# Optimization experiments

Hardware: AMD Instinct MI355X
Metric: run time of the kernel (lower is better)

## Reference

```python
import jax, jax.numpy as jnp
import numpy as np

N = 64000   # nodes
E = 256000  # edges
G = 2000    # graphs
D = 300     # emb_dim
H = 4       # heads
C = D // H  # head dim = 75
L = 5       # layers
ED = 32     # edge_emb_dim
FD = 256    # feat_dim


def _ln(x, g, b):
    m = x.mean(-1, keepdims=True)
    v = jnp.mean((x - m) ** 2, axis=-1, keepdims=True)
    return (x - m) * jax.lax.rsqrt(v + 1e-5) * g + b


def setup_inputs() -> dict:
    key = jax.random.key(0)
    ks = iter(jax.random.split(key, 48))
    def nrm(shape, s=0.02):
        return jax.random.normal(next(ks), shape, jnp.float32) * s
    inp = {}
    inp["x"] = jax.random.randint(next(ks), (N, 2), 0, 3)
    inp["edge_index"] = jax.random.randint(next(ks), (2, E), 0, N)
    inp["edge_attr"] = jax.random.randint(next(ks), (E, 2), 0, 3)
    inp["batch"] = jnp.sort(jax.random.randint(next(ks), (N,), 0, G))
    inp.update(dict(
        x_emb1=nrm((119, D)), x_emb2=nrm((3, D)),
        e_emb_t=nrm((5, ED)), e_emb_d=nrm((3, ED)),
        edge_proj_w=nrm((ED, ED)), edge_proj_b=nrm((ED,)),
        q_w=nrm((L, D, D)), q_b=nrm((L, D)),
        k_w=nrm((L, D, D)), k_b=nrm((L, D)),
        v_w=nrm((L, D, D)), v_b=nrm((L, D)),
        e_w=nrm((L, ED, D)),
        skip_w=nrm((L, D, D)), skip_b=nrm((L, D)),
        ln1_g=jnp.ones((L, D), jnp.float32), ln1_b=jnp.zeros((L, D), jnp.float32),
        ln2_g=jnp.ones((L, D), jnp.float32), ln2_b=jnp.zeros((L, D), jnp.float32),
        ffn_w1=nrm((L, D, 4 * D)), ffn_b1=nrm((L, 4 * D)),
        ffn_w2=nrm((L, 4 * D, D)), ffn_b2=nrm((L, D)),
        feat_w=nrm((D, FD)), feat_b=nrm((FD,)),
        out_w1=nrm((FD, FD)), out_b1=nrm((FD,)),
        out_w2=nrm((FD, FD // 2)), out_b2=nrm((FD // 2,)),
    ))
    return inp


def reference(x, edge_index, edge_attr, batch, x_emb1, x_emb2, e_emb_t, e_emb_d,
              edge_proj_w, edge_proj_b, q_w, q_b, k_w, k_b, v_w, v_b, e_w,
              skip_w, skip_b, ln1_g, ln1_b, ln2_g, ln2_b,
              ffn_w1, ffn_b1, ffn_w2, ffn_b2, feat_w, feat_b,
              out_w1, out_b1, out_w2, out_b2):
    # node / edge embeddings
    h = x_emb1[x[:, 0]] + x_emb2[x[:, 1]]                               # [N, D]
    ef = (e_emb_t[edge_attr[:, 0]] + e_emb_d[edge_attr[:, 1]]) @ edge_proj_w + edge_proj_b  # [E, ED]
    src, dst = edge_index[0], edge_index[1]
    scale = 1.0 / np.sqrt(C).astype(np.float32)
    for l in range(L):  # loop over fixed layer count
        q = (h @ q_w[l] + q_b[l]).reshape(N, H, C)
        k = (h @ k_w[l] + k_b[l]).reshape(N, H, C)
        v = (h @ v_w[l] + v_b[l]).reshape(N, H, C)
        e = (ef @ e_w[l]).reshape(E, H, C)
        kj = k[src] + e                                                 # [E, H, C]
        alpha = jnp.einsum('ehc,ehc->eh', q[dst], kj) * scale           # [E, H]
        amax = jax.lax.stop_gradient(jax.ops.segment_max(alpha, dst, num_segments=N))
        ea = jnp.exp(alpha - amax[dst])
        den = jax.ops.segment_sum(ea, dst, num_segments=N)
        attn = ea / den[dst]                                            # segment softmax over in-edges of dst
        msg = attn[:, :, None] * (v[src] + e)
        agg = jax.ops.segment_sum(msg, dst, num_segments=N).reshape(N, D)
        conv = agg + h @ skip_w[l] + skip_b[l]                          # TransformerConv with root skip
        h = _ln(h + conv, ln1_g[l], ln1_b[l])
        f = jax.nn.relu(h @ ffn_w1[l] + ffn_b1[l]) @ ffn_w2[l] + ffn_b2[l]
        h = _ln(h + f, ln2_g[l], ln2_b[l])
    cnt = jax.ops.segment_sum(jnp.ones((N,), jnp.float32), batch, num_segments=G)
    g = jax.ops.segment_sum(h, batch, num_segments=G) / jnp.clip(cnt, 1.0)[:, None]
    g = g @ feat_w + feat_b                                             # [G, FD]
    out = jax.nn.relu(g @ out_w1 + out_b1) @ out_w2 + out_b2            # [G, FD//2]
    return (g, out)
```

## Files before the change

kernel.cpp:

```cpp
#include <hip/hip_runtime.h>
#include <hip/hip_bf16.h>
#include <math.h>

typedef __hip_bfloat16 bf16;
typedef unsigned short ushort_t;
typedef unsigned int uint_t;

using bf16x8 = __attribute__((ext_vector_type(8))) __bf16;
using f32x4  = __attribute__((ext_vector_type(4))) float;

constexpr int kN  = 64000;
constexpr int kE  = 256000;
constexpr int kG  = 2000;
constexpr int kD  = 300;
constexpr int kH  = 4;
constexpr int kC  = 75;
constexpr int kL  = 5;
constexpr int kED = 32;
constexpr int kFD = 256;
constexpr int kT  = 15;
constexpr int kDp = 320;
constexpr int kKp2 = 1216;
constexpr int kQV = 1280;
constexpr int kQVn = 1264;
constexpr int kOffK = 300, kOffV = 600, kOffS = 900, kOffQE = 1200;
constexpr int kNpW1 = 1280, kNpW2 = 384;
constexpr int kFDp = 304;

static inline int cdiv(int a, int b) { return (a + b - 1) / b; }

__device__ __forceinline__ ushort_t f2bf(float f) {
    uint_t u = __float_as_uint(f);
    uint_t r = u + 0x7FFFu + ((u >> 16) & 1u);
    return (ushort_t)(r >> 16);
}
__device__ __forceinline__ float bu2f(ushort_t u) {
    return __uint_as_float(((uint_t)u) << 16);
}

__device__ __forceinline__ void gld_lds16(const ushort_t* g, ushort_t* l)
{
    __builtin_amdgcn_global_load_lds(
        (const __attribute__((address_space(1))) void*)g,
        (__attribute__((address_space(3))) void*)(uint_t)(unsigned long long)l,
        16, 0, 0);
}

__global__ void detect_kernel(const uint_t* __restrict__ w, int* __restrict__ flag)
{
    if (threadIdx.x == 0 && blockIdx.x == 0)
        *flag = (w[0] == 0x3F803F80u) ? 1 : 0;
}

__global__ void cvt_kernel(const void* __restrict__ in, float* __restrict__ out,
                           long long n, const int* __restrict__ flag)
{
    long long i = (long long)blockIdx.x * 256 + threadIdx.x;
    if (i >= n) return;
    if (*flag) out[i] = bu2f(((const ushort_t*)in)[i]);
    else       out[i] = ((const float*)in)[i];
}

__global__ void out_write_kernel(const float* __restrict__ in, void* __restrict__ out,
                                 long long n, long long eoff, const int* __restrict__ flag)
{
    long long i = (long long)blockIdx.x * 256 + threadIdx.x;
    if (i >= n) return;
    if (*flag) ((bf16*)out)[eoff + i] = __float2bfloat16(in[i]);
    else       ((float*)out)[eoff + i] = in[i];
}

__global__ void wt_kernel(const void* __restrict__ W, long long elemOff,
                          ushort_t* __restrict__ WT,
                          int K, int N, int ldk, const int* __restrict__ flag)
{
    int i = blockIdx.x * 256 + threadIdx.x;
    if (i >= K * N) return;
    int k = i / N, n = i % N;
    ushort_t val;
    if (*flag) val = ((const ushort_t*)W)[elemOff + i];
    else       val = f2bf(((const float*)W)[elemOff + i]);
    WT[(size_t)n * ldk + k] = val;
}

__global__ void biasqkvs_kernel(const float* __restrict__ qb, const float* __restrict__ kb,
                                const float* __restrict__ vb, const float* __restrict__ sb,
                                float* __restrict__ out)
{
    int i = blockIdx.x * 256 + threadIdx.x;
    if (i >= kL * kQV) return;
    int l = i / kQV, c = i % kQV;
    float v = 0.f;
    if (c < kOffK)          v = qb[l * kD + c];
    else if (c < kOffV)     v = kb[l * kD + c - kOffK];
    else if (c < kOffS)     v = vb[l * kD + c - kOffV];
    else if (c < kOffQE)    v = sb[l * kD + c - kOffS];
    out[i] = v;
}

constexpr int gBM = 128, gBN = 128, gBK = 32;
constexpr int kEpiLd = 136;

__global__ __launch_bounds__(256) void mgemm_kernel(
    const ushort_t* __restrict__ A, int lda,
    const ushort_t* __restrict__ BT, int ldb,
    const float* __restrict__ bias,
    ushort_t* __restrict__ outB, int ldob,
    int M, int N, int K, int relu)
{
    __shared__ ushort_t smem[gBM * kEpiLd];
    ushort_t* As = smem;
    ushort_t* Bs = smem + 8192;

    const int tid  = threadIdx.x;

    const int nxg = gridDim.x;
    int bid;
    {
        int nb = nxg * gridDim.y;
        int orig = blockIdx.y * nxg + blockIdx.x;
        int q8 = nb >> 3, r8 = nb & 7;
        int xcd = orig & 7, lid = orig >> 3;
        bid = (xcd < r8 ? xcd * (q8 + 1) : r8 * (q8 + 1) + (xcd - r8) * q8) + lid;
    }
    const int bm = (bid / nxg) * gBM;
    const int bn = (bid % nxg) * gBN;

    const int wave = tid >> 6, lane = tid & 63;
    const int wr = wave >> 1, wc = wave & 1;
    const int lq = lane & 15, qd = lane >> 4;
    const int qs = (qd ^ ((lq >> 1) & 3)) * 8;

    f32x4 acc[4][4];
#pragma unroll
    for (int i = 0; i < 4; i++)
#pragma unroll
        for (int j = 0; j < 4; j++) acc[i][j] = (f32x4){0.f, 0.f, 0.f, 0.f};

    {
#pragma unroll
        for (int p = 0; p < 2; p++) {
            int u = tid + p * 256;
            gld_lds16(A + (size_t)(bm + (u >> 2)) * lda + ((u ^ (u >> 3)) & 3) * 8, As + u * 8);
        }
#pragma unroll
        for (int p = 0; p < 2; p++) {
            int u = tid + p * 256;
            gld_lds16(BT + (size_t)(bn + (u >> 2)) * ldb + ((u ^ (u >> 3)) & 3) * 8, Bs + u * 8);
        }
    }
    __syncthreads();

    const int nk = K / gBK;
    for (int kt = 0; kt < nk; kt++) {
        const int cb = (kt & 1) * 4096;

        bf16x8 af[4], bfg[4];
#pragma unroll
        for (int i = 0; i < 4; i++)
            af[i] = *reinterpret_cast<const bf16x8*>(&As[cb + (wr * 64 + i * 16 + lq) * gBK + qs]);
#pragma unroll
        for (int j = 0; j < 4; j++)
            bfg[j] = *reinterpret_cast<const bf16x8*>(&Bs[cb + (wc * 64 + j * 16 + lq) * gBK + qs]);

        if (kt + 1 < nk) {
            const int k0 = (kt + 1) * gBK;
            const int nb2 = cb ^ 4096;
#pragma unroll
            for (int p = 0; p < 2; p++) {
                int u = tid + p * 256;
                gld_lds16(A + (size_t)(bm + (u >> 2)) * lda + k0 + ((u ^ (u >> 3)) & 3) * 8,
                          As + nb2 + u * 8);
            }
#pragma unroll
            for (int p = 0; p < 2; p++) {
                int u = tid + p * 256;
                gld_lds16(BT + (size_t)(bn + (u >> 2)) * ldb + k0 + ((u ^ (u >> 3)) & 3) * 8,
                          Bs + nb2 + u * 8);
            }
        }

#pragma unroll
        for (int i = 0; i < 4; i++)
#pragma unroll
            for (int j = 0; j < 4; j++)
                acc[i][j] = __builtin_amdgcn_mfma_f32_16x16x32_bf16(af[i], bfg[j], acc[i][j], 0, 0, 0);

        __syncthreads();
    }

#pragma unroll
    for (int i = 0; i < 4; i++) {
#pragma unroll
        for (int j = 0; j < 4; j++) {
            int lcol = wc * 64 + j * 16 + lq;
            int gcol = bn + lcol;
            float bv = (bias && gcol < N) ? bias[gcol] : 0.f;
#pragma unroll
            for (int r2 = 0; r2 < 4; r2++) {
                int lrow = wr * 64 + i * 16 + qd * 4 + r2;
                float v = acc[i][j][r2] + bv;
                if (relu) v = fmaxf(v, 0.f);
                smem[lrow * kEpiLd + lcol] = f2bf(v);
            }
        }
    }
    __syncthreads();
#pragma unroll
    for (int s = 0; s < 8; s++) {
        int seg  = tid + s * 256;
        int lrow = seg >> 4;
        int loff = (seg & 15) * 8;
        int gcol = bn + loff;
        if (gcol + 8 <= ldob) {
            bf16x8 pv = *reinterpret_cast<const bf16x8*>(&smem[lrow * kEpiLd + loff]);
            *reinterpret_cast<bf16x8*>(&outB[(size_t)(bm + lrow) * ldob + gcol]) = pv;
        }
    }
}

__global__ __launch_bounds__(256) void gemm_kernel(
    const float* __restrict__ A, const float* __restrict__ W,
    const float* __restrict__ bias, float* __restrict__ C,
    int M, int N, int K, int relu)
{
    constexpr int BM = 64, BN = 64, BK = 16;
    __shared__ float As[BK][BM + 1];
    __shared__ float Bs[BK][BN + 1];
    const int bm = blockIdx.y * BM;
    const int bn = blockIdx.x * BN;
    const int tid = threadIdx.x;
    const int tr = tid / 16;
    const int tc = tid % 16;
    float acc[4][4] = {};
    for (int k0 = 0; k0 < K; k0 += BK) {
        for (int t = tid; t < BM * BK; t += 256) {
            int r = t / BK, c = t % BK;
            int gr = bm + r, gc = k0 + c;
            As[c][r] = (gr < M && gc < K) ? A[(size_t)gr * K + gc] : 0.f;
        }
        for (int t = tid; t < BK * BN; t += 256) {
            int r = t / BN, c = t % BN;
            int gr = k0 + r, gc = bn + c;
            Bs[r][c] = (gr < K && gc < N) ? W[(size_t)gr * N + gc] : 0.f;
        }
        __syncthreads();
#pragma unroll
        for (int k = 0; k < BK; k++) {
            float a[4], b[4];
#pragma unroll
            for (int i = 0; i < 4; i++) a[i] = As[k][tr * 4 + i];
#pragma unroll
            for (int j = 0; j < 4; j++) b[j] = Bs[k][tc * 4 + j];
#pragma unroll
            for (int i = 0; i < 4; i++)
#pragma unroll
                for (int j = 0; j < 4; j++) acc[i][j] += a[i] * b[j];
        }
        __syncthreads();
    }
#pragma unroll
    for (int i = 0; i < 4; i++) {
        int gr = bm + tr * 4 + i;
        if (gr >= M) continue;
#pragma unroll
        for (int j = 0; j < 4; j++) {
            int gc = bn + tc * 4 + j;
            if (gc >= N) continue;
            float v = acc[i][j];
            if (bias) v += bias[gc];
            if (relu) v = fmaxf(v, 0.f);
            C[(size_t)gr * N + gc] = v;
        }
    }
}

__global__ void node_embed_kernel(const int* __restrict__ x,
                                  const float* __restrict__ emb1,
                                  const float* __restrict__ emb2,
                                  ushort_t* __restrict__ hb)
{
    long long i = (long long)blockIdx.x * blockDim.x + threadIdx.x;
    if (i >= (long long)kN * kD) return;
    int n = (int)(i / kD), d = (int)(i % kD);
    float v = emb1[(size_t)x[n * 2] * kD + d] + emb2[(size_t)x[n * 2 + 1] * kD + d];
    hb[(size_t)n * kDp + d] = f2bf(v);
}

__global__ void eftab_kernel(const float* __restrict__ emb_t, const float* __restrict__ emb_d,
                             const float* __restrict__ pw, const float* __restrict__ pb,
                             float* __restrict__ eftab)
{
    int tid = threadIdx.x;
    if (tid >= kT * kED) return;
    int t = tid / kED, j = tid % kED;
    int a0 = t / 3, a1 = t % 3;
    float acc = pb[j];
#pragma unroll
    for (int k = 0; k < kED; k++) {
        float s = emb_t[a0 * kED + k] + emb_d[a1 * kED + k];
        acc += s * pw[k * kED + j];
    }
    eftab[tid] = acc;
}

__global__ __launch_bounds__(256) void etab_kernel(const float* __restrict__ eftab,
                                                   const float* __restrict__ ew,
                                                   float* __restrict__ etab)
{
    __shared__ float se[kT * kED];
    for (int i = threadIdx.x; i < kT * kED; i += 256) se[i] = eftab[i];
    __syncthreads();
    for (int o = threadIdx.x; o < kT * kD; o += 256) {
        int t = o / kD, d = o % kD;
        float acc = 0.f;
#pragma unroll
        for (int k = 0; k < kED; k++) acc += se[t * kED + k] * ew[k * kD + d];
        etab[o] = acc;
    }
}

__global__ void etabT2_kernel(const float* __restrict__ etab, ushort_t* __restrict__ out)
{
    int i = blockIdx.x * 256 + threadIdx.x;
    if (i >= 64 * kDp) return;
    int j = i / kDp, k = i % kDp;
    ushort_t v = 0;
    if (j < kT * kH && k < kD) {
        int t = j >> 2, hh = j & 3;
        if (k >= hh * kC && k < hh * kC + kC) v = f2bf(etab[t * kD + k]);
    }
    out[i] = v;
}

__global__ void izero_kernel(int* __restrict__ p, int n)
{
    int i = blockIdx.x * 256 + threadIdx.x;
    if (i < n) p[i] = 0;
}

__global__ void deg_kernel(const int* __restrict__ dst, int* __restrict__ deg)
{
    int e = blockIdx.x * 256 + threadIdx.x;
    if (e >= kE) return;
    atomicAdd(&deg[dst[e]], 1);
}

__global__ __launch_bounds__(256) void scan1_kernel(const int* __restrict__ deg, int* __restrict__ bsum)
{
    __shared__ int s[256];
    int i = blockIdx.x * 256 + threadIdx.x;
    s[threadIdx.x] = (i < kN) ? deg[i] : 0;
    __syncthreads();
    for (int off = 128; off > 0; off >>= 1) {
        if (threadIdx.x < off) s[threadIdx.x] += s[threadIdx.x + off];
        __syncthreads();
    }
    if (threadIdx.x == 0) bsum[blockIdx.x] = s[0];
}

__global__ __launch_bounds__(256) void scan2_kernel(const int* __restrict__ bsum, int* __restrict__ boff,
                                                    int nb, int* __restrict__ row_ptr)
{
    __shared__ int s[256];
    int tid = threadIdx.x;
    int v = (tid < nb) ? bsum[tid] : 0;
    s[tid] = v;
    __syncthreads();
    for (int off = 1; off < 256; off <<= 1) {
        int t = (tid >= off) ? s[tid - off] : 0;
        __syncthreads();
        s[tid] += t;
        __syncthreads();
    }
    if (tid < nb) boff[tid] = s[tid] - v;
    if (tid == 255) row_ptr[kN] = s[255];
}

__global__ __launch_bounds__(256) void scan3_kernel(const int* __restrict__ deg, const int* __restrict__ boff,
                                                    int* __restrict__ row_ptr)
{
    __shared__ int s[256];
    int tid = threadIdx.x;
    int i = blockIdx.x * 256 + tid;
    int v = (i < kN) ? deg[i] : 0;
    s[tid] = v;
    __syncthreads();
    for (int off = 1; off < 256; off <<= 1) {
        int t = (tid >= off) ? s[tid - off] : 0;
        __syncthreads();
        s[tid] += t;
        __syncthreads();
    }
    if (i < kN) row_ptr[i] = boff[blockIdx.x] + s[tid] - v;
}

__global__ void poscopy_kernel(const int* __restrict__ row_ptr, int* __restrict__ pos)
{
    int i = blockIdx.x * 256 + threadIdx.x;
    if (i < kN) pos[i] = row_ptr[i];
}

__global__ void fill_kernel(const int* __restrict__ src, const int* __restrict__ dst,
                            const int* __restrict__ edge_attr,
                            int* __restrict__ pos, int* __restrict__ cpack)
{
    int e = blockIdx.x * 256 + threadIdx.x;
    if (e >= kE) return;
    int d = dst[e];
    int slot = atomicAdd(&pos[d], 1);
    cpack[slot] = (src[e] << 8) | (edge_attr[e * 2] * 3 + edge_attr[e * 2 + 1]);
}

__global__ void gptr_kernel(const int* __restrict__ batch, int* __restrict__ gptr)
{
    int i = blockIdx.x * 256 + threadIdx.x;
    if (i >= kN) return;
    int b1 = batch[i];
    int b0 = (i == 0) ? -1 : batch[i - 1];
    for (int g = b0 + 1; g <= b1; g++) gptr[g] = i;
    if (i == kN - 1)
        for (int g = b1 + 1; g <= kG; g++) gptr[g] = kN;
}

__global__ __launch_bounds__(256) void gsln_kernel(
    const int* __restrict__ row_ptr, const int* __restrict__ cpack,
    const ushort_t* __restrict__ qkvs,
    const float* __restrict__ etab,
    const float* __restrict__ g, const float* __restrict__ b,
    ushort_t* __restrict__ hb)
{
    __shared__ float sE[kT * kD];
    for (int i = threadIdx.x; i < kT * kD; i += 256) sE[i] = etab[i];
    __syncthreads();
    const int wslot = threadIdx.x >> 6, lane = threadIdx.x & 63;
    const int hh = lane >> 4, sub = lane & 15;
    const float scale = 0.11547005383792516f;

    int idxj[5];
    bool vj[5];
#pragma unroll
    for (int j = 0; j < 5; j++) {
        int o = sub + 16 * j;
        vj[j] = (o < kC);
        idxj[j] = hh * kC + (vj[j] ? o : 0);
    }

    for (int it = 0; it < 4; it++) {
        int n = blockIdx.x * 4 + wslot + it * 16000;
        int beg = row_ptr[n], end = row_ptr[n + 1];
        const ushort_t* qrow = qkvs + (size_t)n * kQV;

        float qv[5];
#pragma unroll
        for (int j = 0; j < 5; j++)
            qv[j] = vj[j] ? bu2f(qrow[idxj[j]]) : 0.f;

        float acc[5] = {0.f, 0.f, 0.f, 0.f, 0.f};
        float den = 0.f;
        for (int i = beg; i < end; i++) {
            int pk = cpack[i];
            int s = pk >> 8, t = pk & 255;
            const ushort_t* srow = qkvs + (size_t)s * kQV;
            float hp = 0.f;
#pragma unroll
            for (int j = 0; j < 5; j++)
                if (vj[j]) hp += qv[j] * bu2f(srow[kOffK + idxj[j]]);
            hp += __shfl_xor(hp, 1, 64);
            hp += __shfl_xor(hp, 2, 64);
            hp += __shfl_xor(hp, 4, 64);
            hp += __shfl_xor(hp, 8, 64);
            float a = (hp + bu2f(qrow[kOffQE + t * kH + hh])) * scale;
            a = fminf(fmaxf(a, -60.f), 60.f);
            float eh = expf(a);
            den += eh;
            const float* ep = sE + t * kD;
#pragma unroll
            for (int j = 0; j < 5; j++)
                if (vj[j]) acc[j] += eh * (bu2f(srow[kOffV + idxj[j]]) + ep[idxj[j]]);
        }

        const float inv_den = (den > 0.f) ? 1.f / den : 0.f;
        const ushort_t* skipp = qrow + kOffS;
        float vals[5], sum = 0.f;
#pragma unroll
        for (int j = 0; j < 5; j++) {
            float tV = 0.f;
            if (vj[j])
                tV = bu2f(hb[(size_t)n * kDp + idxj[j]]) + acc[j] * inv_den + bu2f(skipp[idxj[j]]);
            vals[j] = tV;
            sum += tV;
        }
        for (int off = 1; off < 64; off <<= 1) sum += __shfl_xor(sum, off, 64);
        float mean = sum / kD;
        float var = 0.f;
#pragma unroll
        for (int j = 0; j < 5; j++) {
            if (vj[j]) { float dv = vals[j] - mean; var += dv * dv; }
        }
        for (int off = 1; off < 64; off <<= 1) var += __shfl_xor(var, off, 64);
        float rstd = rsqrtf(var / kD + 1e-5f);
#pragma unroll
        for (int j = 0; j < 5; j++) {
            if (vj[j])
                hb[(size_t)n * kDp + idxj[j]] =
                    f2bf((vals[j] - mean) * rstd * g[idxj[j]] + b[idxj[j]]);
        }
    }
}

__global__ __launch_bounds__(256) void ln2_kernel(
    ushort_t* hb, const ushort_t* __restrict__ f, int ldf,
    const float* __restrict__ g, const float* __restrict__ b)
{
    int row  = (blockIdx.x * blockDim.x + threadIdx.x) >> 6;
    int lane = threadIdx.x & 63;
    if (row >= kN) return;
    size_t baseH = (size_t)row * kDp;
    size_t baseF = (size_t)row * ldf;
    float vals[5];
    float sum = 0.f;
#pragma unroll
    for (int i = 0; i < 5; i++) {
        int idx = lane + i * 64;
        float t = 0.f;
        if (idx < kD) t = bu2f(hb[baseH + idx]) + bu2f(f[baseF + idx]);
        vals[i] = t;
        sum += t;
    }
    for (int off = 1; off < 64; off <<= 1) sum += __shfl_xor(sum, off, 64);
    float mean = sum / kD;
    float var = 0.f;
#pragma unroll
    for (int i = 0; i < 5; i++) {
        int idx = lane + i * 64;
        if (idx < kD) { float dv = vals[i] - mean; var += dv * dv; }
    }
    for (int off = 1; off < 64; off <<= 1) var += __shfl_xor(var, off, 64);
    float rstd = rsqrtf(var / kD + 1e-5f);
#pragma unroll
    for (int i = 0; i < 5; i++) {
        int idx = lane + i * 64;
        if (idx < kD)
            hb[baseH + idx] = f2bf((vals[i] - mean) * rstd * g[idx] + b[idx]);
    }
}

__global__ void zero_kernel(float* __restrict__ p, long long n)
{
    long long i = (long long)blockIdx.x * blockDim.x + threadIdx.x;
    if (i < n) p[i] = 0.f;
}

__global__ __launch_bounds__(256) void pool2_kernel(const ushort_t* __restrict__ hb,
                                                    const int* __restrict__ gptr,
                                                    float* __restrict__ pooled)
{
    int g = blockIdx.x;
    int beg = gptr[g], end = gptr[g + 1];
    float inv = (end > beg) ? 1.f / (float)(end - beg) : 0.f;
    for (int d = threadIdx.x; d < kD; d += 256) {
        float acc = 0.f;
        for (int n = beg; n < end; n++)
            acc += bu2f(hb[(size_t)n * kDp + d]);
        pooled[(size_t)g * kD + d] = acc * inv;
    }
}

extern "C" void kernel_launch(void* const* d_in, const int* in_sizes, int n_in,
                              void* d_out, int out_size, void* d_ws, size_t ws_size,
                              hipStream_t stream)
{
    const int* x          = (const int*)d_in[0];
    const int* edge_index = (const int*)d_in[1];
    const int* edge_attr  = (const int*)d_in[2];
    const int* batch      = (const int*)d_in[3];
    const int* src = edge_index;
    const int* dst = edge_index + kE;

    float* ws = (float*)d_ws;
    size_t off = 0;
    int* flag = (int*)(ws + off); off += 16;
    const bool big[33] = {false,false,false,false,false,false,false,false,false,false,
                          true, false, true, false, true, false, false, true, false, false,
                          false,false,false, true, false, true, false,false,false,false,
                          false,false,false};
    float* canon[33] = {};
    for (int i = 4; i < 33; i++) {
        if (big[i]) continue;
        canon[i] = ws + off; off += (size_t)in_sizes[i];
    }
    off = (off + 3) & ~(size_t)3;
    int* deg     = (int*)(ws + off); off += (size_t)kN;
    int* row_ptr = (int*)(ws + off); off += (size_t)kN + 4;
    int* pos     = (int*)(ws + off); off += (size_t)kN;
    int* cpack   = (int*)(ws + off); off += (size_t)kE;
    int* bsum    = (int*)(ws + off); off += 256;
    int* boff    = (int*)(ws + off); off += 256;
    int* gptr    = (int*)(ws + off); off += (size_t)kG + 4;
    float* eftab = ws + off; off += (size_t)kT * kED;
    float* etab5 = ws + off; off += (size_t)kL * kT * kD;
    float* bqv5  = ws + off; off += (size_t)kL * kQV;
    off = (off + 3) & ~(size_t)3;
    ushort_t* hb   = (ushort_t*)(ws + off); off += (size_t)kN * kDp / 2;
    ushort_t* QV   = (ushort_t*)(ws + off); off += (size_t)kN * kQV / 2;
    ushort_t* fbuf = (ushort_t*)(ws + off); off += (size_t)kN * kFDp / 2;
    ushort_t* warena = (ushort_t*)(ws + off);
    ushort_t* wqv5 = warena;
    ushort_t* wt15 = wqv5 + (size_t)kL * kQV * kDp;
    ushort_t* wt25 = wt15 + (size_t)kL * kNpW1 * kDp;
    size_t warena_ushorts = (size_t)kL * (kQV + kNpW1) * kDp + (size_t)kL * kNpW2 * kKp2;
    off += warena_ushorts / 2 + 4;
    float* pooled = (float*)QV;
    float* gbuf   = pooled + (size_t)kG * kD;
    float* t1     = gbuf + (size_t)kG * kFD;
    float* o2     = t1 + (size_t)kG * kFD;

    detect_kernel<<<1, 64, 0, stream>>>((const uint_t*)d_in[19], flag);
    for (int i = 4; i < 33; i++) {
        if (big[i]) continue;
        long long n = in_sizes[i];
        cvt_kernel<<<cdiv((int)n, 256), 256, 0, stream>>>(d_in[i], canon[i], n, flag);
    }

    const long long ND = (long long)kN * kD;

    auto mgemm = [&](const ushort_t* A, int lda, const ushort_t* BT, int ldb,
                     const float* bias, ushort_t* outB, int ldob,
                     int M, int N, int K, int relu) {
        dim3 grid(cdiv(N, 128), M / 128);
        mgemm_kernel<<<grid, 256, 0, stream>>>(A, lda, BT, ldb, bias, outB, ldob, M, N, K, relu);
    };
    auto gemm = [&](const float* A, const float* W, const float* bias, float* C,
                    int M, int N, int K, int relu) {
        dim3 grid(cdiv(N, 64), cdiv(M, 64));
        gemm_kernel<<<grid, 256, 0, stream>>>(A, W, bias, C, M, N, K, relu);
    };

    node_embed_kernel<<<cdiv((int)ND, 256), 256, 0, stream>>>(x, canon[4], canon[5], hb);
    eftab_kernel<<<1, 512, 0, stream>>>(canon[6], canon[7], canon[8], canon[9], eftab);

    const int nb = cdiv(kN, 256);
    izero_kernel<<<cdiv(kN, 256), 256, 0, stream>>>(deg, kN);
    deg_kernel<<<cdiv(kE, 256), 256, 0, stream>>>(dst, deg);
    scan1_kernel<<<nb, 256, 0, stream>>>(deg, bsum);
    scan2_kernel<<<1, 256, 0, stream>>>(bsum, boff, nb, row_ptr);
    scan3_kernel<<<nb, 256, 0, stream>>>(deg, boff, row_ptr);
    poscopy_kernel<<<cdiv(kN, 256), 256, 0, stream>>>(row_ptr, pos);
    fill_kernel<<<cdiv(kE, 256), 256, 0, stream>>>(src, dst, edge_attr, pos, cpack);
    gptr_kernel<<<cdiv(kN, 256), 256, 0, stream>>>(batch, gptr);

    zero_kernel<<<cdiv((int)(warena_ushorts / 2), 256) + 1, 256, 0, stream>>>(
        (float*)warena, (long long)(warena_ushorts / 2));
    for (int l = 0; l < kL; l++) {
        ushort_t* wqv = wqv5 + (size_t)l * kQV * kDp;
        ushort_t* w1  = wt15 + (size_t)l * kNpW1 * kDp;
        ushort_t* w2  = wt25 + (size_t)l * kNpW2 * kKp2;
        float* etab   = etab5 + (size_t)l * kT * kD;
        wt_kernel<<<cdiv(kD * kD, 256), 256, 0, stream>>>(d_in[10], (long long)l * kD * kD, wqv, kD, kD, kDp, flag);
        wt_kernel<<<cdiv(kD * kD, 256), 256, 0, stream>>>(d_in[12], (long long)l * kD * kD, wqv + (size_t)kOffK * kDp, kD, kD, kDp, flag);
        wt_kernel<<<cdiv(kD * kD, 256), 256, 0, stream>>>(d_in[14], (long long)l * kD * kD, wqv + (size_t)kOffV * kDp, kD, kD, kDp, flag);
        wt_kernel<<<cdiv(kD * kD, 256), 256, 0, stream>>>(d_in[17], (long long)l * kD * kD, wqv + (size_t)kOffS * kDp, kD, kD, kDp, flag);
        wt_kernel<<<cdiv(kD * 1200, 256), 256, 0, stream>>>(d_in[23], (long long)l * kD * 1200, w1, kD, 1200, kDp, flag);
        wt_kernel<<<cdiv(1200 * kD, 256), 256, 0, stream>>>(d_in[25], (long long)l * 1200 * kD, w2, 1200, kD, kKp2, flag);
        etab_kernel<<<1, 256, 0, stream>>>(eftab, canon[16] + (size_t)l * kED * kD, etab);
        etabT2_kernel<<<cdiv(64 * kDp, 256), 256, 0, stream>>>(etab, wqv + (size_t)kOffQE * kDp);
    }
    biasqkvs_kernel<<<cdiv(kL * kQV, 256), 256, 0, stream>>>(
        canon[11], canon[13], canon[15], canon[18], bqv5);

    for (int l = 0; l < kL; l++) {
        const ushort_t* wqv = wqv5 + (size_t)l * kQV * kDp;
        const ushort_t* w1  = wt15 + (size_t)l * kNpW1 * kDp;
        const ushort_t* w2  = wt25 + (size_t)l * kNpW2 * kKp2;
        const float* etab = etab5 + (size_t)l * kT * kD;

        mgemm(hb, kDp, wqv, kDp, bqv5 + (size_t)l * kQV, QV, kQV, kN, kQVn, kDp, 0);

        gsln_kernel<<<4000, 256, 0, stream>>>(row_ptr, cpack, QV, etab,
            canon[19] + (size_t)l * kD, canon[20] + (size_t)l * kD, hb);

        ushort_t* mid = QV;
        mgemm(hb, kDp, w1, kDp, canon[24] + (size_t)l * 1200, mid, kKp2,
              kN, 1200, kDp, 1);
        mgemm(mid, kKp2, w2, kKp2, canon[26] + (size_t)l * kD, fbuf, kFDp,
              kN, kD, kKp2, 0);

        ln2_kernel<<<kN / 4, 256, 0, stream>>>(hb, fbuf, kFDp,
            canon[21] + (size_t)l * kD, canon[22] + (size_t)l * kD);
    }

    pool2_kernel<<<kG, 256, 0, stream>>>(hb, gptr, pooled);

    gemm(pooled, canon[27], canon[28], gbuf, kG, kFD, kD, 0);
    gemm(gbuf, canon[29], canon[30], t1, kG, kFD, kFD, 1);
    gemm(t1, canon[31], canon[32], o2, kG, kFD / 2, kFD, 0);

    out_write_kernel<<<cdiv(kG * kFD, 256), 256, 0, stream>>>(
        gbuf, d_out, (long long)kG * kFD, 0, flag);
    out_write_kernel<<<cdiv(kG * kFD / 2, 256), 256, 0, stream>>>(
        o2, d_out, (long long)kG * (kFD / 2), (long long)kG * kFD, flag);
}
```

Measured before the change: 2.564 ms.

## Pad head dims to 80 for vectorized gathers and triple-buffer GEMM LDS

Node features are now stored with each head padded from 75 to 80 columns, and the K/V projection columns are reordered to match. The gather/softmax kernel can then load 4 bf16 values at a time and processes two edges per iteration using a faster exp. The MFMA GEMM moves from double to triple-buffered LDS staging, with explicit vmcnt waits and one barrier per k-step. The cost is extra weight-repacking kernels, a slightly wider QKV output, and more LDS per block, which may reduce occupancy.

```diff
diff --git a/kernel.cpp b/kernel.cpp
--- a/kernel.cpp
+++ b/kernel.cpp
@@ -21,9 +21,9 @@
 constexpr int kT  = 15;
 constexpr int kDp = 320;
 constexpr int kKp2 = 1216;
-constexpr int kQV = 1280;
-constexpr int kQVn = 1264;
-constexpr int kOffK = 300, kOffV = 600, kOffS = 900, kOffQE = 1200;
+constexpr int kQV2 = 1304;
+constexpr int kOffK2 = 0, kOffV2 = 320, kOffQ2 = 640, kOffS2 = 940, kOffQE2 = 1240;
+constexpr int kNpQV = 1408;
 constexpr int kNpW1 = 1280, kNpW2 = 384;
 constexpr int kFDp = 304;
 
@@ -36,6 +36,15 @@
 }
 __device__ __forceinline__ float bu2f(ushort_t u) {
     return __uint_as_float(((uint_t)u) << 16);
+}
+__device__ __forceinline__ void up4(uint2 u, float* o) {
+    o[0] = bu2f((ushort_t)(u.x & 0xffffu));
+    o[1] = bu2f((ushort_t)(u.x >> 16));
+    o[2] = bu2f((ushort_t)(u.y & 0xffffu));
+    o[3] = bu2f((ushort_t)(u.y >> 16));
+}
+__device__ __forceinline__ uint_t pk2(float a, float b) {
+    return (uint_t)f2bf(a) | ((uint_t)f2bf(b) << 16);
 }
 
 __device__ __forceinline__ void gld_lds16(const ushort_t* g, ushort_t* l)
@@ -83,18 +92,66 @@
     WT[(size_t)n * ldk + k] = val;
 }
 
+__global__ void wqvfill_kernel(const void* __restrict__ W, long long elemOff,
+                               ushort_t* __restrict__ WT,
+                               int rowBase, int nr, int padN, const int* __restrict__ flag)
+{
+    int i = blockIdx.x * 256 + threadIdx.x;
+    if (i >= nr * kDp) return;
+    int n = i / kDp, k = i - n * kDp;
+    int kh = k / 80, kl = k - kh * 80;
+    int ok = (kl < kC) ? kC * kh + kl : -1;
+    int on = n;
+    if (padN) {
+        int nh = n / 80, nl = n - nh * 80;
+        on = (nl < kC) ? kC * nh + nl : -1;
+    }
+    ushort_t val = 0;
+    if (ok >= 0 && on >= 0) {
+        long long idx = elemOff + (long long)ok * kD + on;
+        if (*flag) val = ((const ushort_t*)W)[idx];
+        else       val = f2bf(((const float*)W)[idx]);
+    }
+    WT[(size_t)(rowBase + n) * kDp + k] = val;
+}
+
+__global__ void wtkp_kernel(const void* __restrict__ W, long long elemOff,
+                            ushort_t* __restrict__ WT,
+                            int N, const int* __restrict__ flag)
+{
+    int i = blockIdx.x * 256 + threadIdx.x;
+    if (i >= N * kDp) return;
+    int n = i / kDp, k = i - n * kDp;
+    int kh = k / 80, kl = k - kh * 80;
+    ushort_t val = 0;
+    if (kl < kC) {
+        long long idx = elemOff + (long long)(kC * kh + kl) * N + n;
+        if (*flag) val = ((const ushort_t*)W)[idx];
+        else       val = f2bf(((const float*)W)[idx]);
+    }
+    WT[(size_t)n * kDp + k] = val;
+}
+
 __global__ void biasqkvs_kernel(const float* __restrict__ qb, const float* __restrict__ kb,
                                 const float* __restrict__ vb, const float* __restrict__ sb,
                                 float* __restrict__ out)
 {
     int i = blockIdx.x * 256 + threadIdx.x;
-    if (i >= kL * kQV) return;
-    int l = i / kQV, c = i % kQV;
+    if (i >= kL * kQV2) return;
+    int l = i / kQV2, c = i - l * kQV2;
     float v = 0.f;
-    if (c < kOffK)          v = qb[l * kD + c];
-    else if (c < kOffV)     v = kb[l * kD + c - kOffK];
-    else if (c < kOffS)     v = vb[l * kD + c - kOffV];
-    else if (c < kOffQE)    v = sb[l * kD + c - kOffS];
+    if (c < kOffV2) {
+        int ch = c / 80, cl = c - ch * 80;
+        if (cl < kC) v = kb[l * kD + kC * ch + cl];
+    } else if (c < kOffQ2) {
+        int c2 = c - kOffV2;
+        int ch = c2 / 80, cl = c2 - ch * 80;
+        if (cl < kC) v = vb[l * kD + kC * ch + cl];
+    } else if (c < kOffS2) {
+        v = qb[l * kD + (c - kOffQ2)];
+    } else if (c < kOffQE2) {
+        v = sb[l * kD + (c - kOffS2)];
+    }
     out[i] = v;
 }
 
@@ -108,9 +165,7 @@
     ushort_t* __restrict__ outB, int ldob,
     int M, int N, int K, int relu)
 {
-    __shared__ ushort_t smem[gBM * kEpiLd];
-    ushort_t* As = smem;
-    ushort_t* Bs = smem + 8192;
+    __shared__ ushort_t smem[3 * 8192];
 
     const int tid  = threadIdx.x;
 
@@ -131,63 +186,58 @@
     const int lq = lane & 15, qd = lane >> 4;
     const int qs = (qd ^ ((lq >> 1) & 3)) * 8;
 
-    f32x4 acc[4][4];
-#pragma unroll
-    for (int i = 0; i < 4; i++)
-#pragma unroll
-        for (int j = 0; j < 4; j++) acc[i][j] = (f32x4){0.f, 0.f, 0.f, 0.f};
-
-    {
+    auto stageAB = [&](int kt, int b) {
+        const int k0 = kt * gBK;
+        ushort_t* dst = smem + b * 8192;
 #pragma unroll
         for (int p = 0; p < 2; p++) {
             int u = tid + p * 256;
-            gld_lds16(A + (size_t)(bm + (u >> 2)) * lda + ((u ^ (u >> 3)) & 3) * 8, As + u * 8);
+            gld_lds16(A + (size_t)(bm + (u >> 2)) * lda + k0 + ((u ^ (u >> 3)) & 3) * 8,
+                      dst + u * 8);
         }
 #pragma unroll
         for (int p = 0; p < 2; p++) {
             int u = tid + p * 256;
-            gld_lds16(BT + (size_t)(bn + (u >> 2)) * ldb + ((u ^ (u >> 3)) & 3) * 8, Bs + u * 8);
-        }
-    }
-    __syncthreads();
+            gld_lds16(BT + (size_t)(bn + (u >> 2)) * ldb + k0 + ((u ^ (u >> 3)) & 3) * 8,
+                      dst + 4096 + u * 8);
+        }
+    };
+
+    f32x4 acc[4][4];
+#pragma unroll
+    for (int i = 0; i < 4; i++)
+#pragma unroll
+        for (int j = 0; j < 4; j++) acc[i][j] = (f32x4){0.f, 0.f, 0.f, 0.f};
 
     const int nk = K / gBK;
+    stageAB(0, 0);
+    if (nk > 1) stageAB(1, 1);
+
     for (int kt = 0; kt < nk; kt++) {
-        const int cb = (kt & 1) * 4096;
+        if (kt + 1 < nk) asm volatile("s_waitcnt vmcnt(4)" ::: "memory");
+        else             asm volatile("s_waitcnt vmcnt(0)" ::: "memory");
+        __builtin_amdgcn_s_barrier();
+        __builtin_amdgcn_sched_barrier(0);
+
+        const ushort_t* cb = smem + (kt % 3) * 8192;
 
         bf16x8 af[4], bfg[4];
 #pragma unroll
         for (int i = 0; i < 4; i++)
-            af[i] = *reinterpret_cast<const bf16x8*>(&As[cb + (wr * 64 + i * 16 + lq) * gBK + qs]);
+            af[i] = *reinterpret_cast<const bf16x8*>(&cb[(wr * 64 + i * 16 + lq) * gBK + qs]);
 #pragma unroll
         for (int j = 0; j < 4; j++)
-            bfg[j] = *reinterpret_cast<const bf16x8*>(&Bs[cb + (wc * 64 + j * 16 + lq) * gBK + qs]);
-
-        if (kt + 1 < nk) {
-            const int k0 = (kt + 1) * gBK;
-            const int nb2 = cb ^ 4096;
-#pragma unroll
-            for (int p = 0; p < 2; p++) {
-                int u = tid + p * 256;
-                gld_lds16(A + (size_t)(bm + (u >> 2)) * lda + k0 + ((u ^ (u >> 3)) & 3) * 8,
-                          As + nb2 + u * 8);
-            }
-#pragma unroll
-            for (int p = 0; p < 2; p++) {
-                int u = tid + p * 256;
-                gld_lds16(BT + (size_t)(bn + (u >> 2)) * ldb + k0 + ((u ^ (u >> 3)) & 3) * 8,
-                          Bs + nb2 + u * 8);
-            }
-        }
+            bfg[j] = *reinterpret_cast<const bf16x8*>(&cb[4096 + (wc * 64 + j * 16 + lq) * gBK + qs]);
+
+        if (kt + 2 < nk) stageAB(kt + 2, (kt + 2) % 3);
 
 #pragma unroll
         for (int i = 0; i < 4; i++)
 #pragma unroll
             for (int j = 0; j < 4; j++)
                 acc[i][j] = __builtin_amdgcn_mfma_f32_16x16x32_bf16(af[i], bfg[j], acc[i][j], 0, 0, 0);
-
-        __syncthreads();
-    }
+    }
+    __syncthreads();
 
 #pragma unroll
     for (int i = 0; i < 4; i++) {
@@ -284,7 +334,8 @@
     if (i >= (long long)kN * kD) return;
     int n = (int)(i / kD), d = (int)(i % kD);
     float v = emb1[(size_t)x[n * 2] * kD + d] + emb2[(size_t)x[n * 2 + 1] * kD + d];
-    hb[(size_t)n * kDp + d] = f2bf(v);
+    int dh = d / kC, dl = d - dh * kC;
+    hb[(size_t)n * kDp + 80 * dh + dl] = f2bf(v);
 }
 
 __global__ void eftab_kernel(const float* __restrict__ emb_t, const float* __restrict__ emb_d,
@@ -324,13 +375,12 @@
 {
     int i = blockIdx.x * 256 + threadIdx.x;
     if (i >= 64 * kDp) return;
-    int j = i / kDp, k = i % kDp;
+    int j = i / kDp, k = i - j * kDp;
+    int t = j >> 2, hh = j & 3;
+    int kh = k / 80, kl = k - kh * 80;
     ushort_t v = 0;
-    if (j < kT * kH && k < kD) {
-        int t = j >> 2, hh = j & 3;
-        if (k >= hh * kC && k < hh * kC + kC) v = f2bf(etab[t * kD + k]);
-    }
-    out[i] = v;
+    if (t < kT && kh == hh && kl < kC) v = f2bf(etab[t * kD + kC * hh + kl]);
+    out[(size_t)j * kDp + k] = v;
 }
 
 __global__ void izero_kernel(int* __restrict__ p, int n)
@@ -430,81 +480,157 @@
     const float* __restrict__ g, const float* __restrict__ b,
     ushort_t* __restrict__ hb)
 {
-    __shared__ float sE[kT * kD];
-    for (int i = threadIdx.x; i < kT * kD; i += 256) sE[i] = etab[i];
+    __shared__ float sEp[kT * kDp];
+    for (int i = threadIdx.x; i < kT * kDp; i += 256) {
+        int t = i / kDp, o = i - t * kDp;
+        int kh = o / 80, kl = o - kh * 80;
+        sEp[i] = (kl < kC) ? etab[t * kD + kC * kh + kl] : 0.f;
+    }
     __syncthreads();
+
     const int wslot = threadIdx.x >> 6, lane = threadIdx.x & 63;
     const int hh = lane >> 4, sub = lane & 15;
+    const bool j1 = (sub < 4);
+    const int e0 = 4 * sub;
+    const int e1 = 64 + 4 * sub;
+    const int hoff0 = 80 * hh + e0;
+    const int hoff1 = 80 * hh + e1;
     const float scale = 0.11547005383792516f;
 
-    int idxj[5];
-    bool vj[5];
-#pragma unroll
-    for (int j = 0; j < 5; j++) {
-        int o = sub + 16 * j;
-        vj[j] = (o < kC);
-        idxj[j] = hh * kC + (vj[j] ? o : 0);
+    bool v1[4];
+#pragma unroll
+    for (int t = 0; t < 4; t++) v1[t] = j1 && (e1 + t < kC);
+
+    float g0[4], b0[4], g1[4], b1[4];
+#pragma unroll
+    for (int t = 0; t < 4; t++) {
+        g0[t] = g[kC * hh + e0 + t];
+        b0[t] = b[kC * hh + e0 + t];
+        g1[t] = v1[t] ? g[kC * hh + e1 + t] : 0.f;
+        b1[t] = v1[t] ? b[kC * hh + e1 + t] : 0.f;
     }
 
     for (int it = 0; it < 4; it++) {
         int n = blockIdx.x * 4 + wslot + it * 16000;
         int beg = row_ptr[n], end = row_ptr[n + 1];
-        const ushort_t* qrow = qkvs + (size_t)n * kQV;
-
-        float qv[5];
-#pragma unroll
-        for (int j = 0; j < 5; j++)
-            qv[j] = vj[j] ? bu2f(qrow[idxj[j]]) : 0.f;
-
-        float acc[5] = {0.f, 0.f, 0.f, 0.f, 0.f};
+        const ushort_t* qrow = qkvs + (size_t)n * kQV2;
+
+        float qv0[4], qv1[4];
+#pragma unroll
+        for (int t = 0; t < 4; t++) {
+            qv0[t] = bu2f(qrow[kOffQ2 + kC * hh + e0 + t]);
+            qv1[t] = v1[t] ? bu2f(qrow[kOffQ2 + kC * hh + e1 + t]) : 0.f;
+        }
+
+        float acc0[4] = {0.f, 0.f, 0.f, 0.f};
+        float acc1[4] = {0.f, 0.f, 0.f, 0.f};
         float den = 0.f;
-        for (int i = beg; i < end; i++) {
-            int pk = cpack[i];
-            int s = pk >> 8, t = pk & 255;
-            const ushort_t* srow = qkvs + (size_t)s * kQV;
-            float hp = 0.f;
-#pragma unroll
-            for (int j = 0; j < 5; j++)
-                if (vj[j]) hp += qv[j] * bu2f(srow[kOffK + idxj[j]]);
-            hp += __shfl_xor(hp, 1, 64);
-            hp += __shfl_xor(hp, 2, 64);
-            hp += __shfl_xor(hp, 4, 64);
-            hp += __shfl_xor(hp, 8, 64);
-            float a = (hp + bu2f(qrow[kOffQE + t * kH + hh])) * scale;
-            a = fminf(fmaxf(a, -60.f), 60.f);
-            float eh = expf(a);
-            den += eh;
-            const float* ep = sE + t * kD;
-#pragma unroll
-            for (int j = 0; j < 5; j++)
-                if (vj[j]) acc[j] += eh * (bu2f(srow[kOffV + idxj[j]]) + ep[idxj[j]]);
+        uint2 kz{};
+        for (int i = beg; i < end; i += 2) {
+            int pk0 = cpack[i];
+            bool h1 = (i + 1 < end);
+            int pk1 = cpack[h1 ? i + 1 : i];
+            int s0 = pk0 >> 8, t0 = pk0 & 255;
+            int s1 = pk1 >> 8, t1 = pk1 & 255;
+            const ushort_t* sr0 = qkvs + (size_t)s0 * kQV2;
+            const ushort_t* sr1 = qkvs + (size_t)s1 * kQV2;
+
+            uint2 ka0 = *(const uint2*)(sr0 + hoff0);
+            uint2 ka1 = *(const uint2*)(sr1 + hoff0);
+            uint2 kb0 = j1 ? *(const uint2*)(sr0 + hoff1) : kz;
+            uint2 kb1 = j1 ? *(const uint2*)(sr1 + hoff1) : kz;
+            uint2 va0 = *(const uint2*)(sr0 + kOffV2 + hoff0);
+            uint2 va1 = *(const uint2*)(sr1 + kOffV2 + hoff0);
+            uint2 vb0 = j1 ? *(const uint2*)(sr0 + kOffV2 + hoff1) : kz;
+            uint2 vb1 = j1 ? *(const uint2*)(sr1 + kOffV2 + hoff1) : kz;
+            float qe0 = bu2f(qrow[kOffQE2 + t0 * kH + hh]);
+            float qe1 = bu2f(qrow[kOffQE2 + t1 * kH + hh]);
+
+            float kf0[4], kf1[4], kg0[4], kg1[4];
+            up4(ka0, kf0); up4(ka1, kf1); up4(kb0, kg0); up4(kb1, kg1);
+            float hp0 = 0.f, hp1 = 0.f;
+#pragma unroll
+            for (int t = 0; t < 4; t++) {
+                hp0 += qv0[t] * kf0[t] + qv1[t] * kg0[t];
+                hp1 += qv0[t] * kf1[t] + qv1[t] * kg1[t];
+            }
+            hp0 += __shfl_xor(hp0, 1, 64);  hp1 += __shfl_xor(hp1, 1, 64);
+            hp0 += __shfl_xor(hp0, 2, 64);  hp1 += __shfl_xor(hp1, 2, 64);
+            hp0 += __shfl_xor(hp0, 4, 64);  hp1 += __shfl_xor(hp1, 4, 64);
+            hp0 += __shfl_xor(hp0, 8, 64);  hp1 += __shfl_xor(hp1, 8, 64);
+            float a0 = fminf(fmaxf((hp0 + qe0) * scale, -60.f), 60.f);
+            float a1 = fminf(fmaxf((hp1 + qe1) * scale, -60.f), 60.f);
+            float eh0 = __expf(a0);
+            float eh1 = h1 ? __expf(a1) : 0.f;
+            den += eh0 + eh1;
+
+            const float* ep0 = sEp + t0 * kDp;
+            const float* ep1 = sEp + t1 * kDp;
+            f32x4 ea0 = *reinterpret_cast<const f32x4*>(ep0 + hoff0);
+            f32x4 ea1 = *reinterpret_cast<const f32x4*>(ep1 + hoff0);
+            float vf0[4], vf1[4], vg0[4], vg1[4];
+            up4(va0, vf0); up4(va1, vf1); up4(vb0, vg0); up4(vb1, vg1);
+#pragma unroll
+            for (int t = 0; t < 4; t++)
+                acc0[t] += eh0 * (vf0[t] + ea0[t]) + eh1 * (vf1[t] + ea1[t]);
+            if (j1) {
+                f32x4 eb0 = *reinterpret_cast<const f32x4*>(ep0 + hoff1);
+                f32x4 eb1 = *reinterpret_cast<const f32x4*>(ep1 + hoff1);
+#pragma unroll
+                for (int t = 0; t < 4; t++)
+                    acc1[t] += eh0 * (vg0[t] + eb0[t]) + eh1 * (vg1[t] + eb1[t]);
+            }
         }
 
         const float inv_den = (den > 0.f) ? 1.f / den : 0.f;
-        const ushort_t* skipp = qrow + kOffS;
-        float vals[5], sum = 0.f;
-#pragma unroll
-        for (int j = 0; j < 5; j++) {
-            float tV = 0.f;
-            if (vj[j])
-                tV = bu2f(hb[(size_t)n * kDp + idxj[j]]) + acc[j] * inv_den + bu2f(skipp[idxj[j]]);
-            vals[j] = tV;
-            sum += tV;
+        ushort_t* hrow = hb + (size_t)n * kDp;
+        uint2 hu0 = *(const uint2*)(hrow + hoff0);
+        uint2 hu1 = j1 ? *(const uint2*)(hrow + hoff1) : kz;
+        float hf0[4], hf1[4];
+        up4(hu0, hf0); up4(hu1, hf1);
+
+        float vals0[4], vals1[4], sum = 0.f;
+#pragma unroll
+        for (int t = 0; t < 4; t++) {
+            float sk = bu2f(qrow[kOffS2 + kC * hh + e0 + t]);
+            vals0[t] = hf0[t] + acc0[t] * inv_den + sk;
+            sum += vals0[t];
+        }
+#pragma unroll
+        for (int t = 0; t < 4; t++) {
+            float tv = 0.f;
+            if (v1[t])
+                tv = hf1[t] + acc1[t] * inv_den + bu2f(qrow[kOffS2 + kC * hh + e1 + t]);
+            vals1[t] = tv;
+            sum += tv;
         }
         for (int off = 1; off < 64; off <<= 1) sum += __shfl_xor(sum, off, 64);
         float mean = sum / kD;
         float var = 0.f;
 #pragma unroll
-        for (int j = 0; j < 5; j++) {
-            if (vj[j]) { float dv = vals[j] - mean; var += dv * dv; }
+        for (int t = 0; t < 4; t++) { float dv = vals0[t] - mean; var += dv * dv; }
+#pragma unroll
+        for (int t = 0; t < 4; t++) {
+            if (v1[t]) { float dv = vals1[t] - mean; var += dv * dv; }
         }
         for (int off = 1; off < 64; off <<= 1) var += __shfl_xor(var, off, 64);
         float rstd = rsqrtf(var / kD + 1e-5f);
-#pragma unroll
-        for (int j = 0; j < 5; j++) {
-            if (vj[j])
-                hb[(size_t)n * kDp + idxj[j]] =
-                    f2bf((vals[j] - mean) * rstd * g[idxj[j]] + b[idxj[j]]);
+
+        float w0[4];
+#pragma unroll
+        for (int t = 0; t < 4; t++) w0[t] = (vals0[t] - mean) * rstd * g0[t] + b0[t];
+        uint2 o0;
+        o0.x = pk2(w0[0], w0[1]);
+        o0.y = pk2(w0[2], w0[3]);
+        *(uint2*)(hrow + hoff0) = o0;
+        if (j1) {
+            float w1v[4];
+#pragma unroll
+            for (int t = 0; t < 4; t++) w1v[t] = (vals1[t] - mean) * rstd * g1[t] + b1[t];
+            uint2 o1;
+            o1.x = pk2(w1v[0], w1v[1]);
+            o1.y = pk2(w1v[2], w1v[3]);
+            *(uint2*)(hrow + hoff1) = o1;
         }
     }
 }
@@ -519,12 +645,17 @@
     size_t baseH = (size_t)row * kDp;
     size_t baseF = (size_t)row * ldf;
     float vals[5];
+    int uns[5];
+    bool vm[5];
     float sum = 0.f;
 #pragma unroll
     for (int i = 0; i < 5; i++) {
         int idx = lane + i * 64;
+        int kh = idx / 80, kl = idx - kh * 80;
+        vm[i] = (kl < kC);
+        uns[i] = kC * kh + kl;
         float t = 0.f;
-        if (idx < kD) t = bu2f(hb[baseH + idx]) + bu2f(f[baseF + idx]);
+        if (vm[i]) t = bu2f(hb[baseH + idx]) + bu2f(f[baseF + uns[i]]);
         vals[i] = t;
         sum += t;
     }
@@ -533,16 +664,17 @@
     float var = 0.f;
 #pragma unroll
     for (int i = 0; i < 5; i++) {
-        int idx = lane + i * 64;
-        if (idx < kD) { float dv = vals[i] - mean; var += dv * dv; }
+        if (vm[i]) { float dv = vals[i] - mean; var += dv * dv; }
     }
     for (int off = 1; off < 64; off <<= 1) var += __shfl_xor(var, off, 64);
     float rstd = rsqrtf(var / kD + 1e-5f);
 #pragma unroll
     for (int i = 0; i < 5; i++) {
         int idx = lane + i * 64;
-        if (idx < kD)
-            hb[baseH + idx] = f2bf((vals[i] - mean) * rstd * g[idx] + b[idx]);
+        if (vm[i])
+            hb[baseH + idx] = f2bf((vals[i] - mean) * rstd * g[uns[i]] + b[uns[i]]);
+        else
+            hb[baseH + idx] = 0;
     }
 }
 
@@ -560,9 +692,11 @@
     int beg = gptr[g], end = gptr[g + 1];
     float inv = (end > beg) ? 1.f / (float)(end - beg) : 0.f;
     for (int d = threadIdx.x; d < kD; d += 256) {
+        int dh = d / kC, dl = d - dh * kC;
+        int srci = 80 * dh + dl;
         float acc = 0.f;
         for (int n = beg; n < end; n++)
-            acc += bu2f(hb[(size_t)n * kDp + d]);
+            acc += bu2f(hb[(size_t)n * kDp + srci]);
         pooled[(size_t)g * kD + d] = acc * inv;
     }
 }
@@ -600,16 +734,16 @@
     int* gptr    = (int*)(ws + off); off += (size_t)kG + 4;
     float* eftab = ws + off; off += (size_t)kT * kED;
     float* etab5 = ws + off; off += (size_t)kL * kT * kD;
-    float* bqv5  = ws + off; off += (size_t)kL * kQV;
+    float* bqv5  = ws + off; off += (size_t)kL * kQV2;
     off = (off + 3) & ~(size_t)3;
     ushort_t* hb   = (ushort_t*)(ws + off); off += (size_t)kN * kDp / 2;
-    ushort_t* QV   = (ushort_t*)(ws + off); off += (size_t)kN * kQV / 2;
+    ushort_t* QV   = (ushort_t*)(ws + off); off += (size_t)kN * kQV2 / 2;
     ushort_t* fbuf = (ushort_t*)(ws + off); off += (size_t)kN * kFDp / 2;
     ushort_t* warena = (ushort_t*)(ws + off);
     ushort_t* wqv5 = warena;
-    ushort_t* wt15 = wqv5 + (size_t)kL * kQV * kDp;
+    ushort_t* wt15 = wqv5 + (size_t)kL * kNpQV * kDp;
     ushort_t* wt25 = wt15 + (size_t)kL * kNpW1 * kDp;
-    size_t warena_ushorts = (size_t)kL * (kQV + kNpW1) * kDp + (size_t)kL * kNpW2 * kKp2;
+    size_t warena_ushorts = (size_t)kL * (kNpQV + kNpW1) * kDp + (size_t)kL * kNpW2 * kKp2;
     off += warena_ushorts / 2 + 4;
     float* pooled = (float*)QV;
     float* gbuf   = pooled + (size_t)kG * kD;
@@ -637,6 +771,8 @@
         gemm_kernel<<<grid, 256, 0, stream>>>(A, W, bias, C, M, N, K, relu);
     };
 
+    zero_kernel<<<cdiv((int)((long long)kN * kDp / 2), 256), 256, 0, stream>>>(
+        (float*)hb, (long long)kN * kDp / 2);
     node_embed_kernel<<<cdiv((int)ND, 256), 256, 0, stream>>>(x, canon[4], canon[5], hb);
     eftab_kernel<<<1, 512, 0, stream>>>(canon[6], canon[7], canon[8], canon[9], eftab);
 
@@ -653,29 +789,30 @@
     zero_kernel<<<cdiv((int)(warena_ushorts / 2), 256) + 1, 256, 0, stream>>>(
         (float*)warena, (long long)(warena_ushorts / 2));
     for (int l = 0; l < kL; l++) {
-        ushort_t* wqv = wqv5 + (size_t)l * kQV * kDp;
+        ushort_t* wqv = wqv5 + (size_t)l * kNpQV * kDp;
         ushort_t* w1  = wt15 + (size_t)l * kNpW1 * kDp;
         ushort_t* w2  = wt25 + (size_t)l * kNpW2 * kKp2;
         float* etab   = etab5 + (size_t)l * kT * kD;
-        wt_kernel<<<cdiv(kD * kD, 256), 256, 0, stream>>>(d_in[10], (long long)l * kD * kD, wqv, kD, kD, kDp, flag);
-        wt_kernel<<<cdiv(kD * kD, 256), 256, 0, stream>>>(d_in[12], (long long)l * kD * kD, wqv + (size_t)kOffK * kDp, kD, kD, kDp, flag);
-        wt_kernel<<<cdiv(kD * kD, 256), 256, 0, stream>>>(d_in[14], (long long)l * kD * kD, wqv + (size_t)kOffV * kDp, kD, kD, kDp, flag);
-        wt_kernel<<<cdiv(kD * kD, 256), 256, 0, stream>>>(d_in[17], (long long)l * kD * kD, wqv + (size_t)kOffS * kDp, kD, kD, kDp, flag);
-        wt_kernel<<<cdiv(kD * 1200, 256), 256, 0, stream>>>(d_in[23], (long long)l * kD * 1200, w1, kD, 1200, kDp, flag);
+        const long long dd = (long long)l * kD * kD;
+        wqvfill_kernel<<<cdiv(320 * kDp, 256), 256, 0, stream>>>(d_in[12], dd, wqv, kOffK2, 320, 1, flag);
+        wqvfill_kernel<<<cdiv(320 * kDp, 256), 256, 0, stream>>>(d_in[14], dd, wqv, kOffV2, 320, 1, flag);
+        wqvfill_kernel<<<cdiv(300 * kDp, 256), 256, 0, stream>>>(d_in[10], dd, wqv, kOffQ2, 300, 0, flag);
+        wqvfill_kernel<<<cdiv(300 * kDp, 256), 256, 0, stream>>>(d_in[17], dd, wqv, kOffS2, 300, 0, flag);
+        wtkp_kernel<<<cdiv(1200 * kDp, 256), 256, 0, stream>>>(d_in[23], (long long)l * kD * 1200, w1, 1200, flag);
         wt_kernel<<<cdiv(1200 * kD, 256), 256, 0, stream>>>(d_in[25], (long long)l * 1200 * kD, w2, 1200, kD, kKp2, flag);
         etab_kernel<<<1, 256, 0, stream>>>(eftab, canon[16] + (size_t)l * kED * kD, etab);
-        etabT2_kernel<<<cdiv(64 * kDp, 256), 256, 0, stream>>>(etab, wqv + (size_t)kOffQE * kDp);
-    }
-    biasqkvs_kernel<<<cdiv(kL * kQV, 256), 256, 0, stream>>>(
+        etabT2_kernel<<<cdiv(64 * kDp, 256), 256, 0, stream>>>(etab, wqv + (size_t)kOffQE2 * kDp);
+    }
+    biasqkvs_kernel<<<cdiv(kL * kQV2, 256), 256, 0, stream>>>(
         canon[11], canon[13], canon[15], canon[18], bqv5);
 
     for (int l = 0; l < kL; l++) {
-        const ushort_t* wqv = wqv5 + (size_t)l * kQV * kDp;
+        const ushort_t* wqv = wqv5 + (size_t)l * kNpQV * kDp;
         const ushort_t* w1  = wt15 + (size_t)l * kNpW1 * kDp;
         const ushort_t* w2  = wt25 + (size_t)l * kNpW2 * kKp2;
         const float* etab = etab5 + (size_t)l * kT * kD;
 
-        mgemm(hb, kDp, wqv, kDp, bqv5 + (size_t)l * kQV, QV, kQV, kN, kQVn, kDp, 0);
+        mgemm(hb, kDp, wqv, kDp, bqv5 + (size_t)l * kQV2, QV, kQV2, kN, kQV2, kDp, 0);
 
         gsln_kernel<<<4000, 256, 0, stream>>>(row_ptr, cpack, QV, etab,
             canon[19] + (size_t)l * kD, canon[20] + (size_t)l * kD, hb);
```

New measurement: 2.961 ms. 15.5% more time.
